# Performance work log

Hardware: AMD Instinct MI355X
Metric: run time of the kernel (lower is better)

Reference implementation:

```python
import jax, jax.numpy as jnp
from jax import lax
import numpy as np

B, T, S, H = 64, 256, 512, 1024  # batch, seq_len, state_size, n_hidden
A, NOUT = 64, 64                 # action_size, n_output
HD = H // 2                      # Dense head width = n_hidden/2


def setup_inputs() -> dict:
    key = jax.random.key(0)
    ks = jax.random.split(key, 10)
    inp = {
        "x": jax.random.normal(ks[0], (B, T, S), dtype=jnp.float32),
        "actions": jax.random.normal(ks[1], (B, A), dtype=jnp.float32),
        "horizon": jax.random.uniform(ks[2], (B, 1), dtype=jnp.float32),
        # LSTM params (Keras gate order i, f, g(cell), o)
        "W_x": jax.random.normal(ks[3], (S, 4 * H), dtype=jnp.float32) * 0.05,
        "W_h": jax.random.normal(ks[4], (H, 4 * H), dtype=jnp.float32) * 0.05,
        "b": jax.random.normal(ks[5], (4 * H,), dtype=jnp.float32) * 0.05,
        # Dense(n_hidden/2, relu)
        "Wd1": jax.random.normal(ks[6], (H, HD), dtype=jnp.float32) * 0.05,
        "bd1": jax.random.normal(ks[7], (HD,), dtype=jnp.float32) * 0.05,
        # output Dense(n_output), input dim = HD + A + 1
        "Wd2": jax.random.normal(ks[8], (HD + A + 1, NOUT), dtype=jnp.float32) * 0.05,
        "bd2": jax.random.normal(ks[9], (NOUT,), dtype=jnp.float32) * 0.05,
    }
    return inp


def _lstm_last_h(x, W_x, W_h, b):
    # Precompute input projection for all timesteps in one big GEMM: [B,T,4H]
    x_proj = jnp.einsum('bts,sg->btg', x, W_x) + b

    def step(carry, xt):
        h, c = carry
        z = xt + h @ W_h                      # [B, 4H]
        i, f, g, o = jnp.split(z, 4, axis=-1)  # Keras gate order i,f,g,o
        i = jax.nn.sigmoid(i)
        f = jax.nn.sigmoid(f)
        g = jnp.tanh(g)
        o = jax.nn.sigmoid(o)
        c = f * c + i * g
        h = o * jnp.tanh(c)
        return (h, c), None

    h0 = jnp.zeros((x.shape[0], W_h.shape[0]), dtype=x.dtype)
    (h, _), _ = lax.scan(step, (h0, h0), jnp.swapaxes(x_proj, 0, 1))
    return h  # final hidden state (return_sequences=False)


def reference(x, actions, horizon, W_x, W_h, b, Wd1, bd1, Wd2, bd2):
    h = _lstm_last_h(x, W_x, W_h, b)                   # [B, H]
    hid = jax.nn.relu(h @ Wd1 + bd1)                   # [B, H/2]
    feat = jnp.concatenate([hid, actions, horizon], 1)  # [B, H/2 + A + 1]
    return feat @ Wd2 + bd2                            # [B, n_output], linear output
```

## Files before the change

kernel.cpp:

```cpp
#include <hip/hip_runtime.h>
#include <stdint.h>

#define NB   64
#define NT   256
#define NS   512
#define NH   1024
#define NG   4096
#define NHD  512
#define NA   64
#define NO   64

typedef float f32x4  __attribute__((ext_vector_type(4)));
typedef short bf16x8 __attribute__((ext_vector_type(8)));
typedef int   i32x4  __attribute__((ext_vector_type(4)));

__device__ __forceinline__ unsigned short f2bf(float f) {
    union { float f; unsigned u; } a; a.f = f;
    unsigned u = a.u;
    return (unsigned short)((u + 0x7fffu + ((u >> 16) & 1u)) >> 16);
}
__device__ __forceinline__ float bf2f(unsigned short h) {
    union { unsigned u; float f; } a; a.u = ((unsigned)h) << 16; return a.f;
}
__device__ __forceinline__ float sigm(float x) {
    return __fdividef(1.0f, 1.0f + __expf(-x));
}
__device__ __forceinline__ float tanh_f(float x) {
    float e = __expf(-2.0f * fabsf(x));
    float r = __fdividef(1.0f - e, 1.0f + e);
    return x >= 0.0f ? r : -r;
}

#define GLD(dst, base, off) \
    asm volatile("global_load_dwordx4 %0, %1, off offset:" #off " sc1" \
                 : "=v"(dst) : "v"(base) : "memory")

#define HKS(WN, ks)                                                              \
    {                                                                            \
        asm volatile("s_waitcnt vmcnt(" #WN ")" : "+v"(q[ks]));                  \
        union { i32x4 i; bf16x8 v; } u0; u0.i = q[ks];                           \
        bf16x8 fh = u0.v;                                                        \
        bf16x8 l0 = whl_lds[w][0][ks][lane];                                     \
        bf16x8 l1 = whl_lds[w][1][ks][lane];                                     \
        bf16x8 l2 = whl_lds[w][2][ks][lane];                                     \
        bf16x8 l3 = whl_lds[w][3][ks][lane];                                     \
        acc[0] = __builtin_amdgcn_mfma_f32_16x16x32_bf16(fh, whh[0][ks], acc[0], 0, 0, 0); \
        acc[1] = __builtin_amdgcn_mfma_f32_16x16x32_bf16(fh, whh[1][ks], acc[1], 0, 0, 0); \
        acc[2] = __builtin_amdgcn_mfma_f32_16x16x32_bf16(fh, whh[2][ks], acc[2], 0, 0, 0); \
        acc[3] = __builtin_amdgcn_mfma_f32_16x16x32_bf16(fh, whh[3][ks], acc[3], 0, 0, 0); \
        acc[0] = __builtin_amdgcn_mfma_f32_16x16x32_bf16(fh, l0, acc[0], 0, 0, 0); \
        acc[1] = __builtin_amdgcn_mfma_f32_16x16x32_bf16(fh, l1, acc[1], 0, 0, 0); \
        acc[2] = __builtin_amdgcn_mfma_f32_16x16x32_bf16(fh, l2, acc[2], 0, 0, 0); \
        acc[3] = __builtin_amdgcn_mfma_f32_16x16x32_bf16(fh, l3, acc[3], 0, 0, 0); \
    }

#define WS_HPK   0
#define WS_HF32  262144
#define WS_HID   524288
#define WS_FLG   655360

__global__ void prologue(unsigned int* __restrict__ hpk32,
                         unsigned int* __restrict__ flg32) {
    int idx = blockIdx.x * blockDim.x + threadIdx.x;
    hpk32[idx] = 0u;
    if (idx < 256) flg32[idx] = 0u;
}

__global__ __launch_bounds__(256, 1) void lstm_persist(
    const float* __restrict__ x, const float* __restrict__ Wx,
    const float* __restrict__ Wh, const float* __restrict__ bias,
    unsigned short* __restrict__ hpack, float* __restrict__ hF32,
    int* __restrict__ flags)
{
    const int g    = blockIdx.x >> 6;
    const int bi   = blockIdx.x & 63;
    const int tid  = threadIdx.x;
    const int w    = tid >> 6;
    const int lane = tid & 63;
    const int lm   = lane & 15;
    const int lq   = lane >> 4;

    __shared__ bf16x8 whl_lds[4][4][8][64];
    __shared__ float zl[4][4][16][17];

    bf16x8 wxh[4][4], wxl[4][4];
    bf16x8 whh[4][8];
    #pragma unroll
    for (int nt = 0; nt < 4; ++nt) {
        const int zc = nt * NH + bi * 16 + lm;
        #pragma unroll
        for (int ks = 0; ks < 4; ++ks)
            #pragma unroll
            for (int j = 0; j < 8; ++j) {
                int k = w * 128 + ks * 32 + lq * 8 + j;
                float v = Wx[(size_t)k * NG + zc];
                unsigned short h = f2bf(v);
                wxh[nt][ks][j] = (short)h;
                wxl[nt][ks][j] = (short)f2bf(v - bf2f(h));
            }
        #pragma unroll
        for (int ks = 0; ks < 8; ++ks) {
            bf16x8 lo;
            #pragma unroll
            for (int j = 0; j < 8; ++j) {
                int k = w * 256 + ks * 32 + lq * 8 + j;
                float v = Wh[(size_t)k * NG + zc];
                unsigned short h = f2bf(v);
                whh[nt][ks][j] = (short)h;
                lo[j] = (short)f2bf(v - bf2f(h));
            }
            whl_lds[w][nt][ks][lane] = lo;
        }
    }

    const int et     = tid & 127;
    const int bloc   = et >> 3;
    const int prc    = et & 7;
    const int gbatch = g * 16 + bloc;
    const int colp   = bi * 16 + prc * 2;
    float bgate[2][4];
    #pragma unroll
    for (int j = 0; j < 2; ++j)
        #pragma unroll
        for (int gt = 0; gt < 4; ++gt)
            bgate[j][gt] = bias[gt * NH + colp + j];
    float c2[2] = {0.0f, 0.0f};

    int* const gflags = flags + g * 64;
    int* const myflag = gflags + bi;
    unsigned int* const hpk32 = reinterpret_cast<unsigned int*>(hpack);

    f32x4 xr[4][2];
    {
        const float* xs = x + (size_t)(g * 16 + lm) * NT * NS + w * 128 + lq * 8;
        #pragma unroll
        for (int ks = 0; ks < 4; ++ks) {
            const f32x4* p = reinterpret_cast<const f32x4*>(xs + ks * 32);
            xr[ks][0] = p[0];
            xr[ks][1] = p[1];
        }
    }

    #pragma unroll 1
    for (int t = 0; t < NT; ++t) {
        if (w == 0) {
            const int* fp = gflags + lane;
            for (;;) {
                int v = __hip_atomic_load(fp, __ATOMIC_RELAXED,
                                          __HIP_MEMORY_SCOPE_AGENT);
                if (__all(v >= t)) break;
                __builtin_amdgcn_s_sleep(1);
            }
        }
        __syncthreads();

        const unsigned short* hb0 = hpack + (size_t)(t & 1) * (NB * NH)
                                  + (size_t)(g * 16 + lm) * NH + w * 256 + lq * 8;
        i32x4 q[8];
        GLD(q[0], hb0, 0);   GLD(q[1], hb0, 64);
        GLD(q[2], hb0, 128); GLD(q[3], hb0, 192);
        GLD(q[4], hb0, 256); GLD(q[5], hb0, 320);
        GLD(q[6], hb0, 384); GLD(q[7], hb0, 448);

        f32x4 acc[4];
        #pragma unroll
        for (int nt = 0; nt < 4; ++nt) {
            acc[nt][0] = 0.f; acc[nt][1] = 0.f;
            acc[nt][2] = 0.f; acc[nt][3] = 0.f;
        }
        #pragma unroll
        for (int ks = 0; ks < 4; ++ks) {
            bf16x8 axh, axl;
            f32x4 vlo = xr[ks][0], vhi = xr[ks][1];
            #pragma unroll
            for (int j = 0; j < 4; ++j) {
                unsigned short h0 = f2bf(vlo[j]);
                axh[j]     = (short)h0;
                axl[j]     = (short)f2bf(vlo[j] - bf2f(h0));
                unsigned short h1 = f2bf(vhi[j]);
                axh[4 + j] = (short)h1;
                axl[4 + j] = (short)f2bf(vhi[j] - bf2f(h1));
            }
            #pragma unroll
            for (int nt = 0; nt < 4; ++nt) {
                acc[nt] = __builtin_amdgcn_mfma_f32_16x16x32_bf16(axh, wxh[nt][ks], acc[nt], 0, 0, 0);
                acc[nt] = __builtin_amdgcn_mfma_f32_16x16x32_bf16(axh, wxl[nt][ks], acc[nt], 0, 0, 0);
                acc[nt] = __builtin_amdgcn_mfma_f32_16x16x32_bf16(axl, wxh[nt][ks], acc[nt], 0, 0, 0);
            }
        }

        HKS(7, 0) HKS(6, 1) HKS(5, 2) HKS(4, 3)
        HKS(3, 4) HKS(2, 5) HKS(1, 6) HKS(0, 7)

        #pragma unroll
        for (int nt = 0; nt < 4; ++nt)
            #pragma unroll
            for (int r = 0; r < 4; ++r)
                zl[w][nt][lq * 4 + r][lm] = acc[nt][r];
        __syncthreads();

        if (tid < 128) {
            float hv[2];
            #pragma unroll
            for (int j = 0; j < 2; ++j) {
                const int n = prc * 2 + j;
                float zg[4];
                #pragma unroll
                for (int gt = 0; gt < 4; ++gt) {
                    zg[gt] = zl[0][gt][bloc][n] + zl[1][gt][bloc][n]
                           + zl[2][gt][bloc][n] + zl[3][gt][bloc][n]
                           + bgate[j][gt];
                }
                float ig = sigm(zg[0]);
                float fg = sigm(zg[1]);
                float gg = tanh_f(zg[2]);
                float og = sigm(zg[3]);
                c2[j] = fg * c2[j] + ig * gg;
                hv[j] = og * tanh_f(c2[j]);
            }
            unsigned pk = (unsigned)f2bf(hv[0]) | ((unsigned)f2bf(hv[1]) << 16);
            const size_t po = (size_t)((t + 1) & 1) * (NB * NH / 2)
                            + (size_t)gbatch * (NH / 2) + bi * 8 + prc;
            __hip_atomic_store(hpk32 + po, pk, __ATOMIC_RELAXED, __HIP_MEMORY_SCOPE_AGENT);
            if (t == NT - 1) {
                hF32[(size_t)gbatch * NH + colp]     = hv[0];
                hF32[(size_t)gbatch * NH + colp + 1] = hv[1];
            }
        }

        __syncthreads();
        if (tid == 0)
            __hip_atomic_store(myflag, t + 1, __ATOMIC_RELAXED, __HIP_MEMORY_SCOPE_AGENT);

        if (t + 1 < NT) {
            const float* xs = x + ((size_t)(g * 16 + lm) * NT + (t + 1)) * NS
                                + w * 128 + lq * 8;
            #pragma unroll
            for (int ks = 0; ks < 4; ++ks) {
                const f32x4* p = reinterpret_cast<const f32x4*>(xs + ks * 32);
                xr[ks][0] = p[0];
                xr[ks][1] = p[1];
            }
        }
    }
}

__global__ void head1(const float* __restrict__ hF32, const float* __restrict__ Wd1,
                      const float* __restrict__ bd1, float* __restrict__ hid)
{
    int b = blockIdx.x >> 1;
    int n = (blockIdx.x & 1) * 256 + threadIdx.x;
    const float* hrow = hF32 + (size_t)b * NH;
    float acc = bd1[n];
    #pragma unroll 4
    for (int k = 0; k < NH; ++k)
        acc += hrow[k] * Wd1[(size_t)k * NHD + n];
    hid[(size_t)b * NHD + n] = fmaxf(acc, 0.0f);
}

__global__ void head2(const float* __restrict__ hid, const float* __restrict__ act,
                      const float* __restrict__ hor, const float* __restrict__ Wd2,
                      const float* __restrict__ bd2, float* __restrict__ out)
{
    int b = blockIdx.x;
    int n = threadIdx.x;
    float acc = bd2[n];
    const float* hrow = hid + (size_t)b * NHD;
    #pragma unroll 4
    for (int k = 0; k < NHD; ++k) acc += hrow[k] * Wd2[(size_t)k * NO + n];
    const float* arow = act + (size_t)b * NA;
    #pragma unroll
    for (int k = 0; k < NA; ++k) acc += arow[k] * Wd2[(size_t)(NHD + k) * NO + n];
    acc += hor[b] * Wd2[(size_t)576 * NO + n];
    out[(size_t)b * NO + n] = acc;
}

extern "C" void kernel_launch(void* const* d_in, const int* in_sizes, int n_in,
                              void* d_out, int out_size, void* d_ws, size_t ws_size,
                              hipStream_t stream)
{
    (void)in_sizes; (void)n_in; (void)out_size; (void)ws_size;
    const float* x    = (const float*)d_in[0];
    const float* act  = (const float*)d_in[1];
    const float* hor  = (const float*)d_in[2];
    const float* Wx   = (const float*)d_in[3];
    const float* Wh   = (const float*)d_in[4];
    const float* bias = (const float*)d_in[5];
    const float* Wd1  = (const float*)d_in[6];
    const float* bd1  = (const float*)d_in[7];
    const float* Wd2  = (const float*)d_in[8];
    const float* bd2  = (const float*)d_in[9];
    float* out = (float*)d_out;

    char* wsb = (char*)d_ws;
    unsigned short* hpk = (unsigned short*)(wsb + WS_HPK);
    float* hF32 = (float*)(wsb + WS_HF32);
    float* hid  = (float*)(wsb + WS_HID);
    int*   flg  = (int*)(wsb + WS_FLG);

    prologue<<<256, 256, 0, stream>>>((unsigned int*)(wsb + WS_HPK),
                                      (unsigned int*)(wsb + WS_FLG));

    lstm_persist<<<dim3(256), dim3(256), 0, stream>>>(x, Wx, Wh, bias,
                                                      hpk, hF32, flg);

    head1<<<128, 256, 0, stream>>>(hF32, Wd1, bd1, hid);
    head2<<<64, 64, 0, stream>>>(hid, act, hor, Wd2, bd2, out);
}
```

Baseline: 1.501 ms.

## Publish per-wave step flags and split head kernels' reductions across threads

Each block now publishes two per-wave progress flags (for waves 0 and 1, the ones writing h) right after their own h stores, replacing the block-wide barrier before a single flag store. Consumers poll both flags with one 64-bit load per lane. This removes a __syncthreads from the recurrent critical path, so waiting blocks can proceed as soon as the producing waves finish. The head kernels are also reshaped: head1 uses one 512-thread block per batch row, and head2 splits its K loop across four waves with an LDS reduction. The per-wave flag protocol relies on s_waitcnt ordering with relaxed atomics, which carries a memory-ordering risk.

```diff
diff --git a/kernel.cpp b/kernel.cpp
--- a/kernel.cpp
+++ b/kernel.cpp
@@ -63,7 +63,7 @@
                          unsigned int* __restrict__ flg32) {
     int idx = blockIdx.x * blockDim.x + threadIdx.x;
     hpk32[idx] = 0u;
-    if (idx < 256) flg32[idx] = 0u;
+    if (idx < 512) flg32[idx] = 0u;
 }
 
 __global__ __launch_bounds__(256, 1) void lstm_persist(
@@ -126,8 +126,8 @@
             bgate[j][gt] = bias[gt * NH + colp + j];
     float c2[2] = {0.0f, 0.0f};
 
-    int* const gflags = flags + g * 64;
-    int* const myflag = gflags + bi;
+    int* const gflags = flags + g * 128;
+    int* const myflag = gflags + bi * 2;
     unsigned int* const hpk32 = reinterpret_cast<unsigned int*>(hpack);
 
     f32x4 xr[4][2];
@@ -144,11 +144,14 @@
     #pragma unroll 1
     for (int t = 0; t < NT; ++t) {
         if (w == 0) {
-            const int* fp = gflags + lane;
+            const unsigned long long* fp =
+                reinterpret_cast<const unsigned long long*>(gflags);
             for (;;) {
-                int v = __hip_atomic_load(fp, __ATOMIC_RELAXED,
-                                          __HIP_MEMORY_SCOPE_AGENT);
-                if (__all(v >= t)) break;
+                unsigned long long v = __hip_atomic_load(fp + lane, __ATOMIC_RELAXED,
+                                                         __HIP_MEMORY_SCOPE_AGENT);
+                int f0 = (int)(v & 0xffffffffu);
+                int f1 = (int)(v >> 32);
+                if (__all(f0 >= t && f1 >= t)) break;
                 __builtin_amdgcn_s_sleep(1);
             }
         }
@@ -226,11 +229,11 @@
                 hF32[(size_t)gbatch * NH + colp]     = hv[0];
                 hF32[(size_t)gbatch * NH + colp + 1] = hv[1];
             }
-        }
-
-        __syncthreads();
-        if (tid == 0)
-            __hip_atomic_store(myflag, t + 1, __ATOMIC_RELAXED, __HIP_MEMORY_SCOPE_AGENT);
+            asm volatile("s_waitcnt vmcnt(0)" ::: "memory");
+            if ((tid & 63) == 0)
+                __hip_atomic_store(myflag + w, t + 1, __ATOMIC_RELAXED,
+                                   __HIP_MEMORY_SCOPE_AGENT);
+        }
 
         if (t + 1 < NT) {
             const float* xs = x + ((size_t)(g * 16 + lm) * NT + (t + 1)) * NS
@@ -245,34 +248,46 @@
     }
 }
 
-__global__ void head1(const float* __restrict__ hF32, const float* __restrict__ Wd1,
-                      const float* __restrict__ bd1, float* __restrict__ hid)
+__global__ __launch_bounds__(512) void head1(
+    const float* __restrict__ hF32, const float* __restrict__ Wd1,
+    const float* __restrict__ bd1, float* __restrict__ hid)
 {
-    int b = blockIdx.x >> 1;
-    int n = (blockIdx.x & 1) * 256 + threadIdx.x;
+    int b = blockIdx.x;
+    int n = threadIdx.x;
     const float* hrow = hF32 + (size_t)b * NH;
     float acc = bd1[n];
-    #pragma unroll 4
+    #pragma unroll 8
     for (int k = 0; k < NH; ++k)
         acc += hrow[k] * Wd1[(size_t)k * NHD + n];
     hid[(size_t)b * NHD + n] = fmaxf(acc, 0.0f);
 }
 
-__global__ void head2(const float* __restrict__ hid, const float* __restrict__ act,
-                      const float* __restrict__ hor, const float* __restrict__ Wd2,
-                      const float* __restrict__ bd2, float* __restrict__ out)
+__global__ __launch_bounds__(256) void head2(
+    const float* __restrict__ hid, const float* __restrict__ act,
+    const float* __restrict__ hor, const float* __restrict__ Wd2,
+    const float* __restrict__ bd2, float* __restrict__ out)
 {
-    int b = blockIdx.x;
-    int n = threadIdx.x;
-    float acc = bd2[n];
+    __shared__ float red[4][64];
+    int b  = blockIdx.x;
+    int n  = threadIdx.x & 63;
+    int ks = threadIdx.x >> 6;
     const float* hrow = hid + (size_t)b * NHD;
+    float acc = 0.0f;
     #pragma unroll 4
-    for (int k = 0; k < NHD; ++k) acc += hrow[k] * Wd2[(size_t)k * NO + n];
-    const float* arow = act + (size_t)b * NA;
-    #pragma unroll
-    for (int k = 0; k < NA; ++k) acc += arow[k] * Wd2[(size_t)(NHD + k) * NO + n];
-    acc += hor[b] * Wd2[(size_t)576 * NO + n];
-    out[(size_t)b * NO + n] = acc;
+    for (int k = ks * 128; k < ks * 128 + 128; ++k)
+        acc += hrow[k] * Wd2[(size_t)k * NO + n];
+    if (ks == 1) {
+        const float* arow = act + (size_t)b * NA;
+        #pragma unroll 4
+        for (int k = 0; k < NA; ++k)
+            acc += arow[k] * Wd2[(size_t)(NHD + k) * NO + n];
+    }
+    if (ks == 2) acc += hor[b] * Wd2[(size_t)576 * NO + n];
+    if (ks == 0) acc += bd2[n];
+    red[ks][n] = acc;
+    __syncthreads();
+    if (threadIdx.x < 64)
+        out[(size_t)b * NO + n] = red[0][n] + red[1][n] + red[2][n] + red[3][n];
 }
 
 extern "C" void kernel_launch(void* const* d_in, const int* in_sizes, int n_in,
@@ -304,6 +319,6 @@
     lstm_persist<<<dim3(256), dim3(256), 0, stream>>>(x, Wx, Wh, bias,
                                                       hpk, hF32, flg);
 
-    head1<<<128, 256, 0, stream>>>(hF32, Wd1, bd1, hid);
-    head2<<<64, 64, 0, stream>>>(hid, act, hor, Wd2, bd2, out);
-}
+    head1<<<64, 512, 0, stream>>>(hF32, Wd1, bd1, hid);
+    head2<<<64, 256, 0, stream>>>(hid, act, hor, Wd2, bd2, out);
+}
```

After: 1.871 ms. 1.25x slower.
